# Kernel optimization log

Hardware: AMD Instinct MI355X
Metric: run time of the kernel (lower is better)

Reference implementation:

```python
import jax, jax.numpy as jnp
import numpy as np

B, C_IN, N_NODES = 512, 128, 511  # padded node axis = N_NODES + 1 (index 0 is the zero vector)


def setup_inputs() -> dict:
    key = jax.random.key(0)
    ks = jax.random.split(key, 8)
    trees = jax.random.normal(ks[0], (B, C_IN, N_NODES + 1), dtype=jnp.float32)
    idxes = jax.random.randint(ks[1], (B, 3 * N_NODES, 1), 0, N_NODES + 1, dtype=jnp.int64)

    def init_conv(k, out_c, in_c):
        kw, kb = jax.random.split(k)
        s = 1.0 / np.sqrt(in_c * 3)
        W = jax.random.uniform(kw, (out_c, in_c, 3), minval=-s, maxval=s, dtype=jnp.float32)
        b = jax.random.uniform(kb, (out_c,), minval=-s, maxval=s, dtype=jnp.float32)
        return W, b

    def init_lin(k, out_c, in_c):
        kw, kb = jax.random.split(k)
        s = 1.0 / np.sqrt(in_c)
        W = jax.random.uniform(kw, (out_c, in_c), minval=-s, maxval=s, dtype=jnp.float32)
        b = jax.random.uniform(kb, (out_c,), minval=-s, maxval=s, dtype=jnp.float32)
        return W, b

    W1, b1 = init_conv(ks[2], 256, C_IN)
    W2, b2 = init_conv(ks[3], 128, 256)
    W3, b3 = init_conv(ks[4], 64, 128)
    Wf1, bf1 = init_lin(ks[5], 32, 64)
    Wf2, bf2 = init_lin(ks[6], 1, 32)
    return dict(trees=trees, idxes=idxes, W1=W1, b1=b1, W2=W2, b2=b2,
                W3=W3, b3=b3, Wf1=Wf1, bf1=bf1, Wf2=Wf2, bf2=bf2)


def _tree_conv(x, idx, W, b):
    # x: [B, C, N+1], idx: [B, 3N] -> gather (self,left,right) triples, conv1d k=3 s=3
    Bs, C, _ = x.shape
    g = jnp.take_along_axis(x, jnp.broadcast_to(idx[:, None, :], (Bs, C, idx.shape[1])), axis=2)
    g = g.reshape(Bs, C, -1, 3)  # [B, C, N, 3]
    out = jnp.einsum('bcnk,ock->bon', g, W) + b[None, :, None]  # [B, O, N]
    zero = jnp.zeros((Bs, out.shape[1], 1), out.dtype)
    return jnp.concatenate([zero, out], axis=2)  # re-add zero-padding node at idx 0


def _tree_norm(x):
    # torch.std is unbiased (ddof=1); normalize over (channel, node) dims per tree
    mean = jnp.mean(x, axis=(1, 2), keepdims=True)
    n = x.shape[1] * x.shape[2]
    var = jnp.sum((x - mean) ** 2, axis=(1, 2), keepdims=True) / (n - 1)
    return (x - mean) / (jnp.sqrt(var) + 1e-5)


def _leaky(x):
    return jnp.where(x >= 0, x, 0.01 * x)


def reference(trees, idxes, W1, b1, W2, b2, W3, b3, Wf1, bf1, Wf2, bf2):
    idx = idxes[..., 0]  # [B, 3N]
    x = _leaky(_tree_norm(_tree_conv(trees, idx, W1, b1)))
    x = _leaky(_tree_norm(_tree_conv(x, idx, W2, b2)))
    x = _tree_norm(_tree_conv(x, idx, W3, b3))
    pooled = jnp.max(x, axis=2)  # DynamicPooling -> [B, 64]
    h = _leaky(pooled @ Wf1.T + bf1)
    return h @ Wf2.T + bf2  # [B, 1]
```

## Files before the change

### kernel.cpp

```cpp
#include <hip/hip_runtime.h>

#define TRIP 1533

typedef __attribute__((ext_vector_type(8))) short bf16x8;
typedef __attribute__((ext_vector_type(4))) float f32x4;

__device__ __forceinline__ void split2(float a, float b, unsigned& h, unsigned& l) {
    unsigned ba = __float_as_uint(a), bb = __float_as_uint(b);
    unsigned ha = ba & 0xFFFF0000u, hb = bb & 0xFFFF0000u;
    float ra = a - __uint_as_float(ha);
    float rb = b - __uint_as_float(hb);
    h = (ba >> 16) | hb;
    l = (__float_as_uint(ra) >> 16) | (__float_as_uint(rb) & 0xFFFF0000u);
}

template<int CIN, int COUT>
__global__ void k_repackW(const float* __restrict__ W,
                          unsigned short* __restrict__ Hi, unsigned short* __restrict__ Lo) {
    int id = blockIdx.x * 256 + threadIdx.x;
    if (id >= 3 * CIN * COUT) return;
    int o = id / (3 * CIN), kk = id % (3 * CIN);
    int ks = kk / CIN, c = kk % CIN;
    float v = W[(o * CIN + c) * 3 + ks];
    unsigned b = __float_as_uint(v);
    unsigned h = b & 0xFFFF0000u;
    float r = v - __uint_as_float(h);
    Hi[id] = (unsigned short)(b >> 16);
    Lo[id] = (unsigned short)(__float_as_uint(r) >> 16);
}

__global__ void k_transpose(const float* __restrict__ in, float* __restrict__ out) {
    __shared__ float tl[64][129];
    int b = blockIdx.z, n0 = blockIdx.x * 64, t = threadIdx.x;
    int n = t & 63;
    for (int c = t >> 6; c < 128; c += 4)
        tl[n][c] = in[((size_t)b * 128 + c) * 512 + n0 + n];
    __syncthreads();
    int cq = t & 31;
    for (int nr = t >> 5; nr < 64; nr += 8) {
        float4 v = { tl[nr][cq*4+0], tl[nr][cq*4+1], tl[nr][cq*4+2], tl[nr][cq*4+3] };
        *(float4*)&out[((size_t)b * 512 + n0 + nr) * 128 + cq * 4] = v;
    }
}

__global__ void k_zero_row0(float* __restrict__ o1, float* __restrict__ o2, float* __restrict__ o3) {
    int b = blockIdx.x, t = threadIdx.x;
    if (t < 256) o1[(size_t)b * 512 * 256 + t] = 0.f;
    if (t < 128) o2[(size_t)b * 512 * 128 + t] = 0.f;
    if (t < 64)  o3[(size_t)b * 512 * 64  + t] = 0.f;
}

template<int CIN, int COUT, bool NORM_IN>
__global__ __launch_bounds__(256, 4) void k_convmfma(
    const float* __restrict__ xin, const int* __restrict__ idx,
    const unsigned short* __restrict__ WHi, const unsigned short* __restrict__ WLo,
    const float* __restrict__ bias, float* __restrict__ out,
    const float* __restrict__ sIn, float* __restrict__ sOut)
{
    constexpr int K  = 3 * CIN;
    constexpr int NK = K / 32;

    __shared__ unsigned short Gh[128][40], Gl[128][40];
    __shared__ unsigned short Wh[64][40],  Wl[64][40];
    __shared__ float rs[4], rq[4];

    const int b    = blockIdx.z;
    const int och0 = blockIdx.y * 64;
    const int n0   = 1 + blockIdx.x * 128;
    const int t    = threadIdx.x;
    const int lane = t & 63, wave = t >> 6;
    const int wm = wave >> 1, wn = wave & 1;
    const int l15 = lane & 15, l16 = lane >> 4;

    float mean = 0.f, inv = 1.f;
    if (NORM_IN) {
        float s = sIn[b * 2], ss = sIn[b * 2 + 1];
        const float nel = (float)(CIN * 512);
        float mu  = s / nel;
        float var = (ss - nel * mu * mu) / (nel - 1.f);
        mean = mu; inv = 1.f / (sqrtf(var) + 1e-5f);
    }

    const int nodeL = t >> 1;
    const int cb    = (t & 1) * 16;
    int il0 = 0, il1 = 0, il2 = 0;
    if (n0 + nodeL <= 511) {
        const int* ip = &idx[b * TRIP + 3 * (n0 - 1 + nodeL)];
        il0 = ip[0]; il1 = ip[1]; il2 = ip[2];
    }
    const float* rowBase = &xin[(size_t)b * 512 * CIN + cb];

    const int wOch = t >> 2, wU = t & 3;
    const unsigned short* wSrcH = &WHi[(size_t)(och0 + wOch) * K + wU * 8];
    const unsigned short* wSrcL = &WLo[(size_t)(och0 + wOch) * K + wU * 8];

    f32x4 acc[4][2] = {};

    float4 g0, g1, g2, g3;
    uint4  wrh, wrl;
    {
        const float* src = rowBase + (size_t)il0 * CIN;
        g0 = *(const float4*)&src[0];  g1 = *(const float4*)&src[4];
        g2 = *(const float4*)&src[8];  g3 = *(const float4*)&src[12];
        wrh = *(const uint4*)&wSrcH[0];
        wrl = *(const uint4*)&wSrcL[0];
    }

    for (int ch = 0; ch < NK; ++ch) {
        __syncthreads();

        {
            float4 v0 = g0, v1 = g1, v2 = g2, v3 = g3;
            if (NORM_IN) {
                #define LKY(x) { x = (x - mean) * inv; x = x >= 0.f ? x : 0.01f * x; }
                LKY(v0.x) LKY(v0.y) LKY(v0.z) LKY(v0.w)
                LKY(v1.x) LKY(v1.y) LKY(v1.z) LKY(v1.w)
                LKY(v2.x) LKY(v2.y) LKY(v2.z) LKY(v2.w)
                LKY(v3.x) LKY(v3.y) LKY(v3.z) LKY(v3.w)
                #undef LKY
            }
            uint4 H0, L0, H1, L1;
            split2(v0.x, v0.y, H0.x, L0.x); split2(v0.z, v0.w, H0.y, L0.y);
            split2(v1.x, v1.y, H0.z, L0.z); split2(v1.z, v1.w, H0.w, L0.w);
            split2(v2.x, v2.y, H1.x, L1.x); split2(v2.z, v2.w, H1.y, L1.y);
            split2(v3.x, v3.y, H1.z, L1.z); split2(v3.z, v3.w, H1.w, L1.w);
            *(uint4*)&Gh[nodeL][cb]     = H0;
            *(uint4*)&Gh[nodeL][cb + 8] = H1;
            *(uint4*)&Gl[nodeL][cb]     = L0;
            *(uint4*)&Gl[nodeL][cb + 8] = L1;
            *(uint4*)&Wh[wOch][wU * 8]  = wrh;
            *(uint4*)&Wl[wOch][wU * 8]  = wrl;
        }

        if (ch + 1 < NK) {
            const int kk0n = (ch + 1) * 32;
            const int ksn  = kk0n / CIN, c0n = kk0n % CIN;
            const int node = ksn == 0 ? il0 : (ksn == 1 ? il1 : il2);
            const float* src = rowBase + (size_t)node * CIN + c0n;
            g0 = *(const float4*)&src[0];  g1 = *(const float4*)&src[4];
            g2 = *(const float4*)&src[8];  g3 = *(const float4*)&src[12];
            wrh = *(const uint4*)&wSrcH[kk0n];
            wrl = *(const uint4*)&wSrcL[kk0n];
        }
        __syncthreads();

        bf16x8 Ah[4], Al[4], Bh[2], Bl[2];
        #pragma unroll
        for (int mi = 0; mi < 4; ++mi) {
            int nl = wm * 64 + mi * 16 + l15;
            Ah[mi] = *(const bf16x8*)&Gh[nl][l16 * 8];
            Al[mi] = *(const bf16x8*)&Gl[nl][l16 * 8];
        }
        #pragma unroll
        for (int ni = 0; ni < 2; ++ni) {
            int ol = wn * 32 + ni * 16 + l15;
            Bh[ni] = *(const bf16x8*)&Wh[ol][l16 * 8];
            Bl[ni] = *(const bf16x8*)&Wl[ol][l16 * 8];
        }
        #pragma unroll
        for (int mi = 0; mi < 4; ++mi)
            #pragma unroll
            for (int ni = 0; ni < 2; ++ni) {
                acc[mi][ni] = __builtin_amdgcn_mfma_f32_16x16x32_bf16(Ah[mi], Bh[ni], acc[mi][ni], 0, 0, 0);
                acc[mi][ni] = __builtin_amdgcn_mfma_f32_16x16x32_bf16(Ah[mi], Bl[ni], acc[mi][ni], 0, 0, 0);
                acc[mi][ni] = __builtin_amdgcn_mfma_f32_16x16x32_bf16(Al[mi], Bh[ni], acc[mi][ni], 0, 0, 0);
            }
    }

    float lsum = 0.f, lss = 0.f;
    #pragma unroll
    for (int ni = 0; ni < 2; ++ni) {
        int ol = wn * 32 + ni * 16 + l15;
        float bi = bias[och0 + ol];
        #pragma unroll
        for (int mi = 0; mi < 4; ++mi) {
            #pragma unroll
            for (int r = 0; r < 4; ++r) {
                int nl = wm * 64 + mi * 16 + l16 * 4 + r;
                int ng = n0 + nl;
                if (ng <= 511) {
                    float v = acc[mi][ni][r] + bi;
                    out[((size_t)b * 512 + ng) * COUT + och0 + ol] = v;
                    lsum += v; lss += v * v;
                }
            }
        }
    }

    #pragma unroll
    for (int off = 32; off > 0; off >>= 1) {
        lsum += __shfl_down(lsum, off);
        lss  += __shfl_down(lss, off);
    }
    if (lane == 0) { rs[wave] = lsum; rq[wave] = lss; }
    __syncthreads();
    if (t == 0) {
        atomicAdd(&sOut[b * 2],     rs[0] + rs[1] + rs[2] + rs[3]);
        atomicAdd(&sOut[b * 2 + 1], rq[0] + rq[1] + rq[2] + rq[3]);
    }
}

__global__ __launch_bounds__(256) void k_pool_fc(
    const float* __restrict__ x,
    const float* __restrict__ stats,
    const float* __restrict__ Wf1, const float* __restrict__ bf1,
    const float* __restrict__ Wf2, const float* __restrict__ bf2,
    float* __restrict__ outp)
{
    __shared__ float cm[4][64];
    __shared__ float pool[64];
    __shared__ float h[32];
    int b = blockIdx.x, t = threadIdx.x;
    int c = t & 63, g = t >> 6;
    float m = -1e30f;
    for (int n = 1 + g; n <= 511; n += 4)
        m = fmaxf(m, x[((size_t)b * 512 + n) * 64 + c]);
    cm[g][c] = m;
    __syncthreads();
    if (t < 64) {
        float mm = fmaxf(fmaxf(cm[0][t], cm[1][t]), fmaxf(cm[2][t], cm[3][t]));
        mm = fmaxf(mm, 0.f);
        float s = stats[b * 2], ss = stats[b * 2 + 1];
        const float nel = 64.f * 512.f;
        float mu  = s / nel;
        float var = (ss - nel * mu * mu) / (nel - 1.f);
        float inv = 1.f / (sqrtf(var) + 1e-5f);
        pool[t] = (mm - mu) * inv;
    }
    __syncthreads();
    if (t < 32) {
        float acc = bf1[t];
        for (int cc = 0; cc < 64; ++cc) acc += pool[cc] * Wf1[t * 64 + cc];
        h[t] = acc >= 0.f ? acc : 0.01f * acc;
    }
    __syncthreads();
    if (t == 0) {
        float acc = bf2[0];
        for (int j = 0; j < 32; ++j) acc += h[j] * Wf2[j];
        outp[b] = acc;
    }
}

extern "C" void kernel_launch(void* const* d_in, const int* in_sizes, int n_in,
                              void* d_out, int out_size, void* d_ws, size_t ws_size,
                              hipStream_t stream)
{
    const float* trees = (const float*)d_in[0];
    const int*   idx32 = (const int*)d_in[1];
    const float* W1  = (const float*)d_in[2];
    const float* b1  = (const float*)d_in[3];
    const float* W2  = (const float*)d_in[4];
    const float* b2  = (const float*)d_in[5];
    const float* W3  = (const float*)d_in[6];
    const float* b3  = (const float*)d_in[7];
    const float* Wf1 = (const float*)d_in[8];
    const float* bf1 = (const float*)d_in[9];
    const float* Wf2 = (const float*)d_in[10];
    const float* bf2 = (const float*)d_in[11];
    float* outp = (float*)d_out;
    char*  ws   = (char*)d_ws;

    float*          stats = (float*)ws;
    unsigned short* w1h = (unsigned short*)(ws + 12288);
    unsigned short* w1l = (unsigned short*)(ws + 208896);
    unsigned short* w2h = (unsigned short*)(ws + 405504);
    unsigned short* w2l = (unsigned short*)(ws + 602112);
    unsigned short* w3h = (unsigned short*)(ws + 798720);
    unsigned short* w3l = (unsigned short*)(ws + 847872);
    char* chunkBase = ws + 897024;
    float* s0 = stats, *s1 = stats + 1024, *s2 = stats + 2048;

    const size_t fixedB = 897024;
    int Bc = 512;
    while (Bc > 1 && fixedB + (size_t)Bc * 917504 > ws_size) Bc >>= 1;

    hipMemsetAsync(stats, 0, 12288, stream);
    k_repackW<128, 256><<<384, 256, 0, stream>>>(W1, w1h, w1l);
    k_repackW<256, 128><<<384, 256, 0, stream>>>(W2, w2h, w2l);
    k_repackW<128, 64><<<96, 256, 0, stream>>>(W3, w3h, w3l);

    float* t0   = (float*)chunkBase;
    float* out1 = (float*)(chunkBase + (size_t)Bc * 262144);
    float* out3 = (float*)(chunkBase + (size_t)Bc * 786432);

    for (int c0 = 0; c0 < 512; c0 += Bc) {
        const float* treesC = trees + (size_t)c0 * 128 * 512;
        const int*   idxC   = idx32 + (size_t)c0 * TRIP;

        k_transpose<<<dim3(8, 1, Bc), 256, 0, stream>>>(treesC, t0);
        k_convmfma<128, 256, false><<<dim3(4, 4, Bc), 256, 0, stream>>>(
            t0, idxC, w1h, w1l, b1, out1, nullptr, s0 + c0 * 2);
        k_zero_row0<<<Bc, 256, 0, stream>>>(out1, t0, out3);
        k_convmfma<256, 128, true><<<dim3(4, 2, Bc), 256, 0, stream>>>(
            out1, idxC, w2h, w2l, b2, t0, s0 + c0 * 2, s1 + c0 * 2);
        k_convmfma<128, 64, true><<<dim3(4, 1, Bc), 256, 0, stream>>>(
            t0, idxC, w3h, w3l, b3, out3, s1 + c0 * 2, s2 + c0 * 2);
        k_pool_fc<<<Bc, 256, 0, stream>>>(out3, s2 + c0 * 2, Wf1, bf1, Wf2, bf2, outp + c0);
    }

    (void)in_sizes; (void)n_in; (void)out_size; (void)ws_size;
}
```

Measured before the change: 725.2 us.

## Widen output-channel tile, double-buffer LDS, and relayout shared tiles

The conv MFMA kernel now takes an output-channel tile size as a template parameter. Layers 1 and 2 use 128 channels per block, which halves how often the same gathered node rows are fetched and split. Shared memory is double-buffered with one barrier per K-chunk, and it uses a k-group-major padded layout so staging the next chunk overlaps the MFMAs. Launch bounds drop to 2 blocks per CU to make room for the larger accumulator and LDS footprint, which lowers occupancy.

```diff
diff --git a/kernel.cpp b/kernel.cpp
--- a/kernel.cpp
+++ b/kernel.cpp
@@ -50,8 +50,8 @@
     if (t < 64)  o3[(size_t)b * 512 * 64  + t] = 0.f;
 }
 
-template<int CIN, int COUT, bool NORM_IN>
-__global__ __launch_bounds__(256, 4) void k_convmfma(
+template<int CIN, int COUT, int OCH_T, bool NORM_IN>
+__global__ __launch_bounds__(256, 2) void k_convmfma(
     const float* __restrict__ xin, const int* __restrict__ idx,
     const unsigned short* __restrict__ WHi, const unsigned short* __restrict__ WLo,
     const float* __restrict__ bias, float* __restrict__ out,
@@ -59,13 +59,17 @@
 {
     constexpr int K  = 3 * CIN;
     constexpr int NK = K / 32;
-
-    __shared__ unsigned short Gh[128][40], Gl[128][40];
-    __shared__ unsigned short Wh[64][40],  Wl[64][40];
+    constexpr int NI = OCH_T / 32;
+    constexpr int OH = OCH_T / 2;
+    constexpr int GP = 128 * 8 + 8;
+    constexpr int WP = OCH_T * 8 + 8;
+
+    __shared__ unsigned short Gh[2 * 4 * GP], Gl[2 * 4 * GP];
+    __shared__ unsigned short Wh[2 * 4 * WP], Wl[2 * 4 * WP];
     __shared__ float rs[4], rq[4];
 
     const int b    = blockIdx.z;
-    const int och0 = blockIdx.y * 64;
+    const int och0 = blockIdx.y * OCH_T;
     const int n0   = 1 + blockIdx.x * 128;
     const int t    = threadIdx.x;
     const int lane = t & 63, wave = t >> 6;
@@ -81,96 +85,113 @@
         mean = mu; inv = 1.f / (sqrtf(var) + 1e-5f);
     }
 
-    const int nodeL = t >> 1;
-    const int cb    = (t & 1) * 16;
+    const int nodeL = t & 127, ghalf = t >> 7, cb = ghalf * 16;
     int il0 = 0, il1 = 0, il2 = 0;
     if (n0 + nodeL <= 511) {
         const int* ip = &idx[b * TRIP + 3 * (n0 - 1 + nodeL)];
         il0 = ip[0]; il1 = ip[1]; il2 = ip[2];
     }
-    const float* rowBase = &xin[(size_t)b * 512 * CIN + cb];
-
-    const int wOch = t >> 2, wU = t & 3;
-    const unsigned short* wSrcH = &WHi[(size_t)(och0 + wOch) * K + wU * 8];
-    const unsigned short* wSrcL = &WLo[(size_t)(och0 + wOch) * K + wU * 8];
-
-    f32x4 acc[4][2] = {};
+    const float* gBase = &xin[(size_t)b * 512 * CIN];
 
     float4 g0, g1, g2, g3;
-    uint4  wrh, wrl;
-    {
-        const float* src = rowBase + (size_t)il0 * CIN;
-        g0 = *(const float4*)&src[0];  g1 = *(const float4*)&src[4];
-        g2 = *(const float4*)&src[8];  g3 = *(const float4*)&src[12];
-        wrh = *(const uint4*)&wSrcH[0];
-        wrl = *(const uint4*)&wSrcL[0];
-    }
+    uint4  wh0, wh1, wl0, wl1;
+
+    auto loadG = [&](int ch) {
+        int ks = (ch * 32) / CIN, c0 = (ch * 32) % CIN;
+        int node = ks == 0 ? il0 : (ks == 1 ? il1 : il2);
+        const float* s = gBase + (size_t)node * CIN + c0 + cb;
+        g0 = *(const float4*)&s[0];  g1 = *(const float4*)&s[4];
+        g2 = *(const float4*)&s[8];  g3 = *(const float4*)&s[12];
+    };
+    auto loadW = [&](int ch) {
+        int kk0 = ch * 32;
+        if constexpr (OCH_T == 128) {
+            const unsigned short* ph = &WHi[(size_t)(och0 + (t & 127)) * K + kk0 + (t >> 7) * 16];
+            const unsigned short* pl = &WLo[(size_t)(och0 + (t & 127)) * K + kk0 + (t >> 7) * 16];
+            wh0 = *(const uint4*)ph; wh1 = *(const uint4*)(ph + 8);
+            wl0 = *(const uint4*)pl; wl1 = *(const uint4*)(pl + 8);
+        } else {
+            const unsigned short* ph = &WHi[(size_t)(och0 + (t & 63)) * K + kk0 + (t >> 6) * 8];
+            const unsigned short* pl = &WLo[(size_t)(och0 + (t & 63)) * K + kk0 + (t >> 6) * 8];
+            wh0 = *(const uint4*)ph;
+            wl0 = *(const uint4*)pl;
+        }
+    };
+    auto stage = [&](int buf) {
+        float4 v0 = g0, v1 = g1, v2 = g2, v3 = g3;
+        if (NORM_IN) {
+            #define LKY(x) { x = (x - mean) * inv; x = x >= 0.f ? x : 0.01f * x; }
+            LKY(v0.x) LKY(v0.y) LKY(v0.z) LKY(v0.w)
+            LKY(v1.x) LKY(v1.y) LKY(v1.z) LKY(v1.w)
+            LKY(v2.x) LKY(v2.y) LKY(v2.z) LKY(v2.w)
+            LKY(v3.x) LKY(v3.y) LKY(v3.z) LKY(v3.w)
+            #undef LKY
+        }
+        uint4 H0, L0, H1, L1;
+        split2(v0.x, v0.y, H0.x, L0.x); split2(v0.z, v0.w, H0.y, L0.y);
+        split2(v1.x, v1.y, H0.z, L0.z); split2(v1.z, v1.w, H0.w, L0.w);
+        split2(v2.x, v2.y, H1.x, L1.x); split2(v2.z, v2.w, H1.y, L1.y);
+        split2(v3.x, v3.y, H1.z, L1.z); split2(v3.z, v3.w, H1.w, L1.w);
+        unsigned short* gh = &Gh[(buf * 4 + 2 * ghalf) * GP + nodeL * 8];
+        unsigned short* gl = &Gl[(buf * 4 + 2 * ghalf) * GP + nodeL * 8];
+        *(uint4*)gh = H0; *(uint4*)(gh + GP) = H1;
+        *(uint4*)gl = L0; *(uint4*)(gl + GP) = L1;
+        if constexpr (OCH_T == 128) {
+            unsigned short* wh = &Wh[(buf * 4 + 2 * ghalf) * WP + nodeL * 8];
+            unsigned short* wl = &Wl[(buf * 4 + 2 * ghalf) * WP + nodeL * 8];
+            *(uint4*)wh = wh0; *(uint4*)(wh + WP) = wh1;
+            *(uint4*)wl = wl0; *(uint4*)(wl + WP) = wl1;
+        } else {
+            unsigned short* wh = &Wh[(buf * 4 + (t >> 6)) * WP + (t & 63) * 8];
+            unsigned short* wl = &Wl[(buf * 4 + (t >> 6)) * WP + (t & 63) * 8];
+            *(uint4*)wh = wh0;
+            *(uint4*)wl = wl0;
+        }
+    };
+
+    f32x4 acc[4][NI] = {};
+
+    loadG(0); loadW(0);
+    stage(0);
+    loadG(1); loadW(1);
+    __syncthreads();
 
     for (int ch = 0; ch < NK; ++ch) {
-        __syncthreads();
-
-        {
-            float4 v0 = g0, v1 = g1, v2 = g2, v3 = g3;
-            if (NORM_IN) {
-                #define LKY(x) { x = (x - mean) * inv; x = x >= 0.f ? x : 0.01f * x; }
-                LKY(v0.x) LKY(v0.y) LKY(v0.z) LKY(v0.w)
-                LKY(v1.x) LKY(v1.y) LKY(v1.z) LKY(v1.w)
-                LKY(v2.x) LKY(v2.y) LKY(v2.z) LKY(v2.w)
-                LKY(v3.x) LKY(v3.y) LKY(v3.z) LKY(v3.w)
-                #undef LKY
-            }
-            uint4 H0, L0, H1, L1;
-            split2(v0.x, v0.y, H0.x, L0.x); split2(v0.z, v0.w, H0.y, L0.y);
-            split2(v1.x, v1.y, H0.z, L0.z); split2(v1.z, v1.w, H0.w, L0.w);
-            split2(v2.x, v2.y, H1.x, L1.x); split2(v2.z, v2.w, H1.y, L1.y);
-            split2(v3.x, v3.y, H1.z, L1.z); split2(v3.z, v3.w, H1.w, L1.w);
-            *(uint4*)&Gh[nodeL][cb]     = H0;
-            *(uint4*)&Gh[nodeL][cb + 8] = H1;
-            *(uint4*)&Gl[nodeL][cb]     = L0;
-            *(uint4*)&Gl[nodeL][cb + 8] = L1;
-            *(uint4*)&Wh[wOch][wU * 8]  = wrh;
-            *(uint4*)&Wl[wOch][wU * 8]  = wrl;
-        }
-
+        const int cur = ch & 1;
         if (ch + 1 < NK) {
-            const int kk0n = (ch + 1) * 32;
-            const int ksn  = kk0n / CIN, c0n = kk0n % CIN;
-            const int node = ksn == 0 ? il0 : (ksn == 1 ? il1 : il2);
-            const float* src = rowBase + (size_t)node * CIN + c0n;
-            g0 = *(const float4*)&src[0];  g1 = *(const float4*)&src[4];
-            g2 = *(const float4*)&src[8];  g3 = *(const float4*)&src[12];
-            wrh = *(const uint4*)&wSrcH[kk0n];
-            wrl = *(const uint4*)&wSrcL[kk0n];
-        }
-        __syncthreads();
-
-        bf16x8 Ah[4], Al[4], Bh[2], Bl[2];
+            stage(cur ^ 1);
+            if (ch + 2 < NK) { loadG(ch + 2); loadW(ch + 2); }
+        }
+        bf16x8 Ah[4], Al[4], Bh[NI], Bl[NI];
+        const unsigned short* ga = &Gh[(cur * 4 + l16) * GP + (wm * 64 + l15) * 8];
+        const unsigned short* gb = &Gl[(cur * 4 + l16) * GP + (wm * 64 + l15) * 8];
         #pragma unroll
         for (int mi = 0; mi < 4; ++mi) {
-            int nl = wm * 64 + mi * 16 + l15;
-            Ah[mi] = *(const bf16x8*)&Gh[nl][l16 * 8];
-            Al[mi] = *(const bf16x8*)&Gl[nl][l16 * 8];
-        }
+            Ah[mi] = *(const bf16x8*)(ga + mi * 128);
+            Al[mi] = *(const bf16x8*)(gb + mi * 128);
+        }
+        const unsigned short* wa = &Wh[(cur * 4 + l16) * WP + (wn * OH + l15) * 8];
+        const unsigned short* wb = &Wl[(cur * 4 + l16) * WP + (wn * OH + l15) * 8];
         #pragma unroll
-        for (int ni = 0; ni < 2; ++ni) {
-            int ol = wn * 32 + ni * 16 + l15;
-            Bh[ni] = *(const bf16x8*)&Wh[ol][l16 * 8];
-            Bl[ni] = *(const bf16x8*)&Wl[ol][l16 * 8];
+        for (int ni = 0; ni < NI; ++ni) {
+            Bh[ni] = *(const bf16x8*)(wa + ni * 128);
+            Bl[ni] = *(const bf16x8*)(wb + ni * 128);
         }
         #pragma unroll
         for (int mi = 0; mi < 4; ++mi)
             #pragma unroll
-            for (int ni = 0; ni < 2; ++ni) {
+            for (int ni = 0; ni < NI; ++ni) {
                 acc[mi][ni] = __builtin_amdgcn_mfma_f32_16x16x32_bf16(Ah[mi], Bh[ni], acc[mi][ni], 0, 0, 0);
                 acc[mi][ni] = __builtin_amdgcn_mfma_f32_16x16x32_bf16(Ah[mi], Bl[ni], acc[mi][ni], 0, 0, 0);
                 acc[mi][ni] = __builtin_amdgcn_mfma_f32_16x16x32_bf16(Al[mi], Bh[ni], acc[mi][ni], 0, 0, 0);
             }
+        __syncthreads();
     }
 
     float lsum = 0.f, lss = 0.f;
     #pragma unroll
-    for (int ni = 0; ni < 2; ++ni) {
-        int ol = wn * 32 + ni * 16 + l15;
+    for (int ni = 0; ni < NI; ++ni) {
+        int ol = wn * OH + ni * 16 + l15;
         float bi = bias[och0 + ol];
         #pragma unroll
         for (int mi = 0; mi < 4; ++mi) {
@@ -288,12 +309,12 @@
         const int*   idxC   = idx32 + (size_t)c0 * TRIP;
 
         k_transpose<<<dim3(8, 1, Bc), 256, 0, stream>>>(treesC, t0);
-        k_convmfma<128, 256, false><<<dim3(4, 4, Bc), 256, 0, stream>>>(
+        k_convmfma<128, 256, 128, false><<<dim3(4, 2, Bc), 256, 0, stream>>>(
             t0, idxC, w1h, w1l, b1, out1, nullptr, s0 + c0 * 2);
         k_zero_row0<<<Bc, 256, 0, stream>>>(out1, t0, out3);
-        k_convmfma<256, 128, true><<<dim3(4, 2, Bc), 256, 0, stream>>>(
+        k_convmfma<256, 128, 128, true><<<dim3(4, 1, Bc), 256, 0, stream>>>(
             out1, idxC, w2h, w2l, b2, t0, s0 + c0 * 2, s1 + c0 * 2);
-        k_convmfma<128, 64, true><<<dim3(4, 1, Bc), 256, 0, stream>>>(
+        k_convmfma<128, 64, 64, true><<<dim3(4, 1, Bc), 256, 0, stream>>>(
             t0, idxC, w3h, w3l, b3, out3, s1 + c0 * 2, s2 + c0 * 2);
         k_pool_fc<<<Bc, 256, 0, stream>>>(out3, s2 + c0 * 2, Wf1, bf1, Wf2, bf2, outp + c0);
     }
```

Result: slower. 930.3 us (+28.3%).
